# Kernel tuning notes

Measured on AMD Instinct MI355X. Metric: run time of the kernel, lower is better.

The kernel has to match this reference:

```python
import jax, jax.numpy as jnp
import numpy as np

S, B, E, H = 2048, 4, 1024, 16

def setup_inputs() -> dict:
    key = jax.random.key(0)
    k1, k2, k3 = jax.random.split(key, 3)
    x = jax.random.normal(k1, (S, B, E), dtype=jnp.float32)
    # xavier-style scale for stable softmax
    in_proj_w = jax.random.normal(k2, (3 * E, E), dtype=jnp.float32) * (1.0 / np.sqrt(E))
    in_proj_b = jnp.zeros((3 * E,), dtype=jnp.float32)
    out_proj_w = jax.random.normal(k3, (E, E), dtype=jnp.float32) * (1.0 / np.sqrt(E))
    out_proj_b = jnp.zeros((E,), dtype=jnp.float32)
    return {"x": x, "in_proj_w": in_proj_w, "in_proj_b": in_proj_b,
            "out_proj_w": out_proj_w, "out_proj_b": out_proj_b, "num_heads": H}


def reference(x, in_proj_w, in_proj_b, out_proj_w, out_proj_b, num_heads):
    # self-attention path: q==k==v -> single fused in-projection
    tgt_len, bsz, embed_dim = x.shape
    head_dim = embed_dim // num_heads
    scaling = float(head_dim) ** -0.5

    qkv = x @ in_proj_w.T + in_proj_b                      # [S, B, 3E]
    q, k, v = jnp.split(qkv, 3, axis=-1)                   # each [S, B, E]
    q = q * scaling

    def to_bhsd(t):
        # [S, B, E] -> [B, H, S, hd]
        return t.reshape(tgt_len, bsz, num_heads, head_dim).transpose(1, 2, 0, 3)

    q, k, v = to_bhsd(q), to_bhsd(k), to_bhsd(v)

    scores = jnp.einsum("bhqd,bhkd->bhqk", q, k)           # [B, H, S, S]
    attn = jax.nn.softmax(scores, axis=-1)                 # dropout_p = 0.0
    out = jnp.einsum("bhqk,bhkd->bhqd", attn, v)           # [B, H, S, hd]

    # [B, H, S, hd] -> [S, B, E]
    out = out.transpose(2, 0, 1, 3).reshape(tgt_len, bsz, embed_dim)
    attn_output = out @ out_proj_w.T + out_proj_b

    # attn weights returned as [B*H, S, S] to match torch layout
    attn_weights = attn.reshape(bsz * num_heads, tgt_len, tgt_len)
    return attn_output, attn_weights
```

## Files before the change

### kernel.cpp

```cpp
#include <hip/hip_runtime.h>

#define S_LEN 2048

typedef __attribute__((ext_vector_type(8))) short short8;
typedef __attribute__((ext_vector_type(4))) float f32x4;
typedef __attribute__((ext_vector_type(2))) unsigned int u32x2;
typedef unsigned short u16;
typedef unsigned int u32;
typedef __attribute__((ext_vector_type(4))) unsigned short us4;

__device__ __forceinline__ u16 f2bf(float f) {
  union { float f; u32 u; } v; v.f = f;
  u32 r = v.u + 0x7FFFu + ((v.u >> 16) & 1u);
  return (u16)(r >> 16);
}

__device__ __forceinline__ u32 cvtpk(float lo, float hi) {
  u32 r;
  asm("v_cvt_pk_bf16_f32 %0, %1, %2" : "=v"(r) : "v"(lo), "v"(hi));
  return r;
}

__device__ __forceinline__ void gload_lds16(const u16* g, u16* l) {
  __builtin_amdgcn_global_load_lds(
      (const __attribute__((address_space(1))) u32*)g,
      (__attribute__((address_space(3))) u32*)l, 16, 0, 0);
}

__device__ __forceinline__ f32x4 mfma16(short8 a, short8 b, f32x4 c) {
  return __builtin_amdgcn_mfma_f32_16x16x32_bf16(a, b, c, 0, 0, 0);
}

template <int NL>
__device__ __forceinline__ void stage8(const u16* __restrict__ gbase, int row_stride,
                                       u16* lds, int tid) {
#pragma unroll
  for (int p = 0; p < NL; ++p) {
    int L = tid + p * 256;
    int r = L >> 3, up = L & 7;
    int u = up ^ (r & 7);
    gload_lds16(gbase + (size_t)r * row_stride + u * 8, lds + (size_t)L * 8);
  }
}
__device__ __forceinline__ short8 ldsfrag8(const u16* lds, int row, int u) {
  int up = u ^ (row & 7);
  return *(const short8*)(lds + (size_t)row * 64 + up * 8);
}

__global__ __launch_bounds__(256) void convert_kernel(
    const float* __restrict__ x, const float* __restrict__ wi, const float* __restrict__ wo,
    u16* __restrict__ xbf, u16* __restrict__ wibf, u16* __restrict__ wobf) {
  int idx = blockIdx.x * 256 + threadIdx.x;
  const float* src; u16* dst; int off;
  if (idx < 2097152)            { src = x;  dst = xbf;  off = idx; }
  else if (idx < 2883584)       { src = wi; dst = wibf; off = idx - 2097152; }
  else                          { src = wo; dst = wobf; off = idx - 2883584; }
  f32x4 v = *(const f32x4*)(src + (size_t)off * 4);
  us4 r;
#pragma unroll
  for (int j = 0; j < 4; ++j) r[j] = f2bf(v[j]);
  *(us4*)(dst + (size_t)off * 4) = r;
}

__device__ __forceinline__ void gemm_core(const u16* __restrict__ A, const u16* __restrict__ B,
                                          int m0, int n0, int K,
                                          u16* aL, u16* bL, f32x4 acc[4][4]) {
  const int tid = threadIdx.x;
  const int lane = tid & 63, w = tid >> 6;
  const int l15 = lane & 15, g = lane >> 4;
  const int wr = w >> 1, wc = w & 1;
#pragma unroll
  for (int i = 0; i < 4; ++i)
#pragma unroll
    for (int n = 0; n < 4; ++n) acc[i][n] = (f32x4){0.f, 0.f, 0.f, 0.f};
  const int nK = K >> 6;
  stage8<4>(A + (size_t)m0 * K, K, aL, tid);
  stage8<4>(B + (size_t)n0 * K, K, bL, tid);
  __syncthreads();
  int buf = 0;
  for (int kt = 0; kt < nK; ++kt) {
    if (kt + 1 < nK) {
      stage8<4>(A + (size_t)m0 * K + (kt + 1) * 64, K, aL + (buf ^ 1) * 8192, tid);
      stage8<4>(B + (size_t)n0 * K + (kt + 1) * 64, K, bL + (buf ^ 1) * 8192, tid);
    }
    const u16* ab = aL + buf * 8192;
    const u16* bb = bL + buf * 8192;
#pragma unroll
    for (int ks = 0; ks < 2; ++ks) {
      short8 af[4], bf[4];
#pragma unroll
      for (int i = 0; i < 4; ++i) af[i] = ldsfrag8(ab, wr * 64 + i * 16 + l15, ks * 4 + g);
#pragma unroll
      for (int n = 0; n < 4; ++n) bf[n] = ldsfrag8(bb, wc * 64 + n * 16 + l15, ks * 4 + g);
      __builtin_amdgcn_s_setprio(1);
#pragma unroll
      for (int i = 0; i < 4; ++i)
#pragma unroll
        for (int n = 0; n < 4; ++n)
          acc[i][n] = mfma16(af[i], bf[n], acc[i][n]);
      __builtin_amdgcn_s_setprio(0);
    }
    __syncthreads();
    buf ^= 1;
  }
}

__device__ __forceinline__ void xcd_remap(int& m0, int& n0) {
  int nM = gridDim.x, nN = gridDim.y;
  int id = blockIdx.y * nM + blockIdx.x;
  int xcd = id & 7, local = id >> 3;
  int mt = xcd * (nM >> 3) + local / nN;
  int nt = local % nN;
  m0 = mt * 128;
  n0 = nt * 128;
}

__global__ __launch_bounds__(256, 2) void gemm_qkv_kernel(
    const u16* __restrict__ xbf, const u16* __restrict__ wbf,
    const float* __restrict__ bias, u16* __restrict__ qkv, u16* __restrict__ vt) {
  __shared__ u16 pool[32768];
  f32x4 acc[4][4];
  int m0, n0;
  xcd_remap(m0, n0);
  gemm_core(xbf, wbf, m0, n0, 1024, pool, pool + 16384, acc);
  const int tid = threadIdx.x, lane = tid & 63, w = tid >> 6;
  const int l15 = lane & 15, g = lane >> 4;
  const int wr = w >> 1, wc = w & 1;
  const int sec = n0 >> 10;
  const float scale = (sec == 0) ? 0.18033688011112042f : 1.0f;
  u16* cl = pool;
#pragma unroll
  for (int n = 0; n < 4; ++n) {
    int c = wc * 64 + n * 16 + l15;
    float bv = bias[n0 + c];
#pragma unroll
    for (int i = 0; i < 4; ++i)
#pragma unroll
      for (int j = 0; j < 4; ++j) {
        int mrow = wr * 64 + i * 16 + g * 4 + j;
        cl[mrow * 132 + c] = f2bf((acc[i][n][j] + bv) * scale);
      }
  }
  __syncthreads();
  const int h0 = (n0 & 1023) >> 6;
  if (sec < 2) {
    u16* dst = qkv + (size_t)sec * 8388608;
#pragma unroll
    for (int rep = 0; rep < 8; ++rep) {
      int chunk = rep * 256 + tid;
      int mrow = chunk >> 4, c = (chunk & 15) << 3;
      short8 vv = *(const short8*)(cl + mrow * 132 + c);
      int mg = m0 + mrow;
      int s = mg >> 2, b = mg & 3;
      int h = h0 + (c >> 6), d = c & 63;
      *(short8*)(dst + (((size_t)(b * 16 + h)) * 2048 + s) * 64 + d) = vv;
    }
  } else {
#pragma unroll
    for (int rep = 0; rep < 8; ++rep) {
      int chunk = rep * 256 + tid;
      int col = chunk >> 4;
      int b = (chunk >> 2) & 3;
      int sc = (chunk & 3) << 3;
      short8 vv;
#pragma unroll
      for (int t = 0; t < 8; ++t)
        vv[t] = (short)cl[(((sc + t) << 2) | b) * 132 + col];
      int h = h0 + (col >> 6), d = col & 63;
      *(short8*)(vt + (size_t)(b * 16 + h) * 131072 + (size_t)d * 2048 + (m0 >> 2) + sc) = vv;
    }
  }
}

__global__ __launch_bounds__(256, 3) void attn_kernel(
    const u16* __restrict__ qkv, const u16* __restrict__ vt,
    float* __restrict__ attn, u16* __restrict__ ows) {
  __shared__ u16 lds[24576];
  const int tid = threadIdx.x, w = tid >> 6, lane = tid & 63;
  const int l15 = lane & 15, g = lane >> 4;
  const int id = blockIdx.y * gridDim.x + blockIdx.x;
  const int xcd = id & 7, t = id >> 3;
  const int bh = xcd * 8 + (t >> 4);
  const int qb = t & 15;
  const int q0 = qb * 128;
  const u16* qbase = qkv + (size_t)bh * 131072;
  const u16* kbase = qkv + 8388608 + (size_t)bh * 131072;
  const u16* vtb = vt + (size_t)bh * 131072;

  short8 qf[2][2];
#pragma unroll
  for (int i = 0; i < 2; ++i)
#pragma unroll
    for (int ks = 0; ks < 2; ++ks)
      qf[i][ks] = *(const short8*)(qbase + ((size_t)(q0 + w * 32 + i * 16 + l15)) * 64 + ks * 32 + g * 8);

  u16* const pw = lds + 16384 + w * 2048;
  float lsum[2] = {0.f, 0.f};
  f32x4 oacc[2][4];
#pragma unroll
  for (int i = 0; i < 2; ++i)
#pragma unroll
    for (int nd = 0; nd < 4; ++nd) oacc[i][nd] = (f32x4){0.f, 0.f, 0.f, 0.f};
  stage8<2>(kbase, 64, lds, tid);
  stage8<2>(vtb, 2048, lds + 8192, tid);
  __syncthreads();
  int buf = 0;
  for (int kt = 0; kt < 32; ++kt) {
    const u16* kb = lds + buf * 4096;
    const u16* vb = lds + 8192 + buf * 4096;
    if (kt < 31) {
      stage8<2>(kbase + (size_t)(kt + 1) * 4096, 64, lds + (buf ^ 1) * 4096, tid);
      stage8<2>(vtb + (size_t)(kt + 1) * 64, 2048, lds + 8192 + (buf ^ 1) * 4096, tid);
    }
    f32x4 acc[2][4];
#pragma unroll
    for (int i = 0; i < 2; ++i)
#pragma unroll
      for (int n = 0; n < 4; ++n) acc[i][n] = (f32x4){0.f, 0.f, 0.f, 0.f};
#pragma unroll
    for (int ks = 0; ks < 2; ++ks) {
      short8 kf[4];
#pragma unroll
      for (int n = 0; n < 4; ++n) kf[n] = ldsfrag8(kb, n * 16 + l15, ks * 4 + g);
      __builtin_amdgcn_s_setprio(1);
#pragma unroll
      for (int i = 0; i < 2; ++i)
#pragma unroll
        for (int n = 0; n < 4; ++n)
          acc[i][n] = mfma16(kf[n], qf[i][ks], acc[i][n]);
      __builtin_amdgcn_s_setprio(0);
    }
#pragma unroll
    for (int i = 0; i < 2; ++i) {
      const int m = i * 16 + l15;
      f32x4 vs = {0.f, 0.f, 0.f, 0.f};
#pragma unroll
      for (int n = 0; n < 4; ++n) {
        f32x4 p4;
        p4[0] = __builtin_amdgcn_exp2f(acc[i][n][0]);
        p4[1] = __builtin_amdgcn_exp2f(acc[i][n][1]);
        p4[2] = __builtin_amdgcn_exp2f(acc[i][n][2]);
        p4[3] = __builtin_amdgcn_exp2f(acc[i][n][3]);
        vs += p4;
        u32x2 pk2;
        pk2[0] = cvtpk(p4[0], p4[1]);
        pk2[1] = cvtpk(p4[2], p4[3]);
        const int up = (n * 2 + (g >> 1)) ^ (m & 7);
        *(u32x2*)(pw + m * 64 + up * 8 + (g & 1) * 4) = pk2;
      }
      float s = (vs[0] + vs[1]) + (vs[2] + vs[3]);
      s += __shfl_xor(s, 16);
      s += __shfl_xor(s, 32);
      lsum[i] += s;
    }
#pragma unroll
    for (int kp = 0; kp < 2; ++kp) {
      short8 ap[2], vf[4];
#pragma unroll
      for (int i = 0; i < 2; ++i) {
        int row = i * 16 + l15;
        ap[i] = *(const short8*)(pw + row * 64 + (((kp * 4 + g) ^ (row & 7)) * 8));
      }
#pragma unroll
      for (int nd = 0; nd < 4; ++nd) vf[nd] = ldsfrag8(vb, nd * 16 + l15, kp * 4 + g);
      __builtin_amdgcn_s_setprio(1);
#pragma unroll
      for (int i = 0; i < 2; ++i)
#pragma unroll
        for (int nd = 0; nd < 4; ++nd)
          oacc[i][nd] = mfma16(ap[i], vf[nd], oacc[i][nd]);
      __builtin_amdgcn_s_setprio(0);
    }
    __syncthreads();
    buf ^= 1;
  }
  float rl[2] = {1.0f / lsum[0], 1.0f / lsum[1]};

  {
    const int b = bh >> 4, h = bh & 15;
#pragma unroll
    for (int i = 0; i < 2; ++i) {
      float rlj[4];
#pragma unroll
      for (int j = 0; j < 4; ++j) rlj[j] = __shfl(rl[i], g * 4 + j);
#pragma unroll
      for (int nd = 0; nd < 4; ++nd)
#pragma unroll
        for (int j = 0; j < 4; ++j) {
          int qrow = q0 + w * 32 + i * 16 + g * 4 + j;
          int d = nd * 16 + l15;
          ows[((size_t)qrow * 4 + b) * 1024 + (size_t)h * 64 + d] =
              f2bf(oacc[i][nd][j] * rlj[j]);
        }
    }
  }

  float linit[2] = {-__log2f(lsum[0]), -__log2f(lsum[1])};

  stage8<4>(kbase, 64, lds, tid);
  __syncthreads();
  buf = 0;
  float* arow = attn + ((size_t)bh * 2048 + q0 + w * 32) * 2048;
  for (int kt = 0; kt < 16; ++kt) {
    if (kt < 15) stage8<4>(kbase + (size_t)(kt + 1) * 8192, 64, lds + (buf ^ 1) * 8192, tid);
    const u16* kb = lds + buf * 8192;
    f32x4 acc[2][8];
#pragma unroll
    for (int i = 0; i < 2; ++i)
#pragma unroll
      for (int n = 0; n < 8; ++n)
        acc[i][n] = (f32x4){linit[i], linit[i], linit[i], linit[i]};
#pragma unroll
    for (int ks = 0; ks < 2; ++ks) {
      short8 kf[8];
#pragma unroll
      for (int n = 0; n < 8; ++n) kf[n] = ldsfrag8(kb, n * 16 + l15, ks * 4 + g);
      __builtin_amdgcn_s_setprio(1);
#pragma unroll
      for (int i = 0; i < 2; ++i)
#pragma unroll
        for (int n = 0; n < 8; ++n)
          acc[i][n] = mfma16(kf[n], qf[i][ks], acc[i][n]);
      __builtin_amdgcn_s_setprio(0);
    }
#pragma unroll
    for (int i = 0; i < 2; ++i) {
      const int m = i * 16 + l15;
#pragma unroll
      for (int n = 0; n < 8; ++n) {
        f32x4 p4;
        p4[0] = __builtin_amdgcn_exp2f(acc[i][n][0]);
        p4[1] = __builtin_amdgcn_exp2f(acc[i][n][1]);
        p4[2] = __builtin_amdgcn_exp2f(acc[i][n][2]);
        p4[3] = __builtin_amdgcn_exp2f(acc[i][n][3]);
        *(f32x4*)(arow + (size_t)m * 2048 + kt * 128 + n * 16 + g * 4) = p4;
      }
    }
    __syncthreads();
    buf ^= 1;
  }
}

__global__ __launch_bounds__(256, 2) void gemm_out_kernel(
    const u16* __restrict__ abf, const u16* __restrict__ wbf,
    const float* __restrict__ bias, float* __restrict__ out) {
  __shared__ u16 pool[32768];
  f32x4 acc[4][4];
  int m0, n0;
  xcd_remap(m0, n0);
  gemm_core(abf, wbf, m0, n0, 1024, pool, pool + 16384, acc);
  const int tid = threadIdx.x, lane = tid & 63, w = tid >> 6;
  const int l15 = lane & 15, g = lane >> 4;
  const int wr = w >> 1, wc = w & 1;
#pragma unroll
  for (int n = 0; n < 4; ++n) {
    int ng = n0 + wc * 64 + n * 16 + l15;
    float bv = bias[ng];
#pragma unroll
    for (int i = 0; i < 4; ++i)
#pragma unroll
      for (int j = 0; j < 4; ++j) {
        int mg = m0 + wr * 64 + i * 16 + g * 4 + j;
        out[(size_t)mg * 1024 + ng] = acc[i][n][j] + bv;
      }
  }
}

extern "C" void kernel_launch(void* const* d_in, const int* in_sizes, int n_in,
                              void* d_out, int out_size, void* d_ws, size_t ws_size,
                              hipStream_t stream) {
  const float* x     = (const float*)d_in[0];
  const float* w_in  = (const float*)d_in[1];
  const float* b_in  = (const float*)d_in[2];
  const float* w_out = (const float*)d_in[3];
  const float* b_out = (const float*)d_in[4];
  float* out  = (float*)d_out;
  float* attn = out + 8388608;

  char* ws = (char*)d_ws;
  u16* qkv  = (u16*)ws;
  u16* vt   = (u16*)(ws + 50331648);
  u16* xbf  = (u16*)(ws + 67108864);
  u16* wibf = (u16*)(ws + 83886080);
  u16* wobf = (u16*)(ws + 90177536);
  u16* ows  = xbf;

  convert_kernel<<<12288, 256, 0, stream>>>(x, w_in, w_out, xbf, wibf, wobf);
  gemm_qkv_kernel<<<dim3(64, 24), 256, 0, stream>>>(xbf, wibf, b_in, qkv, vt);
  attn_kernel<<<dim3(16, 64), 256, 0, stream>>>(qkv, vt, attn, ows);
  gemm_out_kernel<<<dim3(64, 8), 256, 0, stream>>>(ows, wobf, b_out, out);
}
```

Before: 373.6 us.

## Split attention into stats pass and fused tail with out-projection GEMM

```diff
diff --git a/kernel.cpp b/kernel.cpp
--- a/kernel.cpp
+++ b/kernel.cpp
@@ -172,9 +172,9 @@
   }
 }
 
-__global__ __launch_bounds__(256, 3) void attn_kernel(
+__global__ __launch_bounds__(256, 3) void attn_pass1_kernel(
     const u16* __restrict__ qkv, const u16* __restrict__ vt,
-    float* __restrict__ attn, u16* __restrict__ ows) {
+    u16* __restrict__ ows, float* __restrict__ linit_ws) {
   __shared__ u16 lds[24576];
   const int tid = threadIdx.x, w = tid >> 6, lane = tid & 63;
   const int l15 = lane & 15, g = lane >> 4;
@@ -294,16 +294,69 @@
         }
     }
   }
-
-  float linit[2] = {-__log2f(lsum[0]), -__log2f(lsum[1])};
-
-  stage8<4>(kbase, 64, lds, tid);
+  if (g == 0) {
+#pragma unroll
+    for (int i = 0; i < 2; ++i)
+      linit_ws[(size_t)bh * 2048 + q0 + w * 32 + i * 16 + l15] = -__log2f(lsum[i]);
+  }
+}
+
+__global__ __launch_bounds__(256, 2) void tail_kernel(
+    const u16* __restrict__ qkv, const float* __restrict__ linit_ws,
+    const u16* __restrict__ ows, const u16* __restrict__ wobf,
+    const float* __restrict__ bias, float* __restrict__ out,
+    float* __restrict__ attn) {
+  __shared__ u16 pool[32768];
+  const int tid = threadIdx.x, w = tid >> 6, lane = tid & 63;
+  const int l15 = lane & 15, g = lane >> 4;
+  const int id = blockIdx.x;
+  if (id < 512) {
+    const int xcd = id & 7, local = id >> 3;
+    const int m0 = (xcd * 8 + (local >> 3)) * 128;
+    const int n0 = (local & 7) * 128;
+    f32x4 acc[4][4];
+    gemm_core(ows, wobf, m0, n0, 1024, pool, pool + 16384, acc);
+    const int wr = w >> 1, wc = w & 1;
+#pragma unroll
+    for (int n = 0; n < 4; ++n) {
+      int ng = n0 + wc * 64 + n * 16 + l15;
+      float bv = bias[ng];
+#pragma unroll
+      for (int i = 0; i < 4; ++i)
+#pragma unroll
+        for (int j = 0; j < 4; ++j) {
+          int mg = m0 + wr * 64 + i * 16 + g * 4 + j;
+          out[(size_t)mg * 1024 + ng] = acc[i][n][j] + bv;
+        }
+    }
+    return;
+  }
+  const int id2 = id - 512;
+  const int xcd = id2 & 7, t = id2 >> 3;
+  const int bh = xcd * 8 + (t >> 4);
+  const int qb = t & 15;
+  const int q0 = qb * 128;
+  const u16* qbase = qkv + (size_t)bh * 131072;
+  const u16* kbase = qkv + 8388608 + (size_t)bh * 131072;
+
+  short8 qf[2][2];
+#pragma unroll
+  for (int i = 0; i < 2; ++i)
+#pragma unroll
+    for (int ks = 0; ks < 2; ++ks)
+      qf[i][ks] = *(const short8*)(qbase + ((size_t)(q0 + w * 32 + i * 16 + l15)) * 64 + ks * 32 + g * 8);
+  float linit[2];
+#pragma unroll
+  for (int i = 0; i < 2; ++i)
+    linit[i] = linit_ws[(size_t)bh * 2048 + q0 + w * 32 + i * 16 + l15];
+
+  stage8<4>(kbase, 64, pool, tid);
   __syncthreads();
-  buf = 0;
+  int buf = 0;
   float* arow = attn + ((size_t)bh * 2048 + q0 + w * 32) * 2048;
   for (int kt = 0; kt < 16; ++kt) {
-    if (kt < 15) stage8<4>(kbase + (size_t)(kt + 1) * 8192, 64, lds + (buf ^ 1) * 8192, tid);
-    const u16* kb = lds + buf * 8192;
+    if (kt < 15) stage8<4>(kbase + (size_t)(kt + 1) * 8192, 64, pool + (buf ^ 1) * 8192, tid);
+    const u16* kb = pool + buf * 8192;
     f32x4 acc[2][8];
 #pragma unroll
     for (int i = 0; i < 2; ++i)
@@ -338,31 +391,6 @@
     }
     __syncthreads();
     buf ^= 1;
-  }
-}
-
-__global__ __launch_bounds__(256, 2) void gemm_out_kernel(
-    const u16* __restrict__ abf, const u16* __restrict__ wbf,
-    const float* __restrict__ bias, float* __restrict__ out) {
-  __shared__ u16 pool[32768];
-  f32x4 acc[4][4];
-  int m0, n0;
-  xcd_remap(m0, n0);
-  gemm_core(abf, wbf, m0, n0, 1024, pool, pool + 16384, acc);
-  const int tid = threadIdx.x, lane = tid & 63, w = tid >> 6;
-  const int l15 = lane & 15, g = lane >> 4;
-  const int wr = w >> 1, wc = w & 1;
-#pragma unroll
-  for (int n = 0; n < 4; ++n) {
-    int ng = n0 + wc * 64 + n * 16 + l15;
-    float bv = bias[ng];
-#pragma unroll
-    for (int i = 0; i < 4; ++i)
-#pragma unroll
-      for (int j = 0; j < 4; ++j) {
-        int mg = m0 + wr * 64 + i * 16 + g * 4 + j;
-        out[(size_t)mg * 1024 + ng] = acc[i][n][j] + bv;
-      }
   }
 }
 
@@ -378,15 +406,16 @@
   float* attn = out + 8388608;
 
   char* ws = (char*)d_ws;
-  u16* qkv  = (u16*)ws;
-  u16* vt   = (u16*)(ws + 50331648);
-  u16* xbf  = (u16*)(ws + 67108864);
-  u16* wibf = (u16*)(ws + 83886080);
-  u16* wobf = (u16*)(ws + 90177536);
-  u16* ows  = xbf;
+  u16* qkv   = (u16*)ws;
+  u16* vt    = (u16*)(ws + 50331648);
+  u16* xbf   = (u16*)(ws + 67108864);
+  u16* wibf  = (u16*)(ws + 83886080);
+  u16* wobf  = (u16*)(ws + 90177536);
+  float* lin = (float*)(ws + 92274688);
+  u16* ows   = xbf;
 
   convert_kernel<<<12288, 256, 0, stream>>>(x, w_in, w_out, xbf, wibf, wobf);
   gemm_qkv_kernel<<<dim3(64, 24), 256, 0, stream>>>(xbf, wibf, b_in, qkv, vt);
-  attn_kernel<<<dim3(16, 64), 256, 0, stream>>>(qkv, vt, attn, ows);
-  gemm_out_kernel<<<dim3(64, 8), 256, 0, stream>>>(ows, wobf, b_out, out);
-}
+  attn_pass1_kernel<<<dim3(16, 64), 256, 0, stream>>>(qkv, vt, ows, lin);
+  tail_kernel<<<1536, 256, 0, stream>>>(qkv, lin, ows, wobf, b_out, out, attn);
+}
```

Result: no change. 378.9 us (+1.4%).
